# Optimization experiments

Measured on AMD Instinct MI355X. Metric: run time of the kernel, lower is better.

Reference implementation:

```python
import jax, jax.numpy as jnp
import numpy as np

RES = 4096
MAX_VAL = 1.0
COST_SCALE = 0.01
WIDTH = 11
N_ITERS = 20


def setup_inputs() -> dict:
    key = jax.random.key(0)
    k1, k2, k3, k4 = jax.random.split(key, 4)
    x = jax.random.uniform(k1, (RES, RES), jnp.float32)
    bt = jax.random.randint(k2, (RES, RES), 1, 3).astype(jnp.float32)
    sparse = (jax.random.uniform(k4, (RES, RES)) < 0.01).astype(jnp.float32)
    boundary_types = bt * sparse
    boundary_conditions = jax.random.uniform(k3, (RES, RES), jnp.float32) * MAX_VAL
    C = COST_SCALE * jnp.ones((RES, RES), jnp.float32)
    return {"x": x, "boundary_types": boundary_types,
            "boundary_conditions": boundary_conditions, "C": C}


def _neighbor_avg(V):
    # 5-point Jacobi stencil average with edge-replicate boundary handling
    Vp = jnp.pad(V, 1, mode='edge')
    return 0.25 * (Vp[:-2, 1:-1] + Vp[2:, 1:-1] + Vp[1:-1, :-2] + Vp[1:-1, 2:])


def reference(x, boundary_types, boundary_conditions, C):
    obj = boundary_types > 0
    V0 = jnp.where(obj, boundary_conditions, x)
    C_pos = jax.nn.relu(C)

    # dilate object boundary values with a uniform width x width box filter
    objects_bounds = boundary_conditions * (boundary_types == 1) * (boundary_conditions > 0)
    w = jnp.full((1, 1, WIDTH, WIDTH), 1.0 / (WIDTH * WIDTH), jnp.float32)
    extra = jax.lax.conv_general_dilated(
        objects_bounds[None, None], w, window_strides=(1, 1), padding='SAME')[0, 0]
    extra = extra * (boundary_types == 0)
    Cc = C_pos + extra  # effective cost field, shape (RES, RES)

    interior = boundary_types == 0

    def step(V, _):
        Vn = jnp.where(interior, _neighbor_avg(V) + Cc, boundary_conditions)
        return Vn, None

    V, _ = jax.lax.scan(step, V0, None, length=N_ITERS)

    out = jnp.where(V >= MAX_VAL, 0.95 * MAX_VAL, V)
    out = jnp.where(obj, boundary_conditions, out)
    return (out, C_pos)
```

## Files before the change

### kernel.cpp

```cpp
#include <hip/hip_runtime.h>
#include <cstdint>

#define RES 4096
#define N_CELLS (RES*RES)

#define T_STEPS 5
#define OW 64
#define OH 64
#define HALO_V 5
#define HALO_H 8
#define IW (OW + 2*HALO_H)
#define IH (OH + 2*HALO_V)
#define NF4 (IW/4)
#define NSLOT (NF4*IH)
#define NTHR 512
#define LDSW IW
#define BUFSZ (IH*LDSW + 8)
#define K2_LIM (NSLOT - 2*NTHR)

__device__ __forceinline__ void jstep(const float* __restrict__ src,
                                      float* __restrict__ dst,
                                      int lo, int gr, int gc, uint4 pk)
{
    const float4 ctr = *(const float4*)(src + lo);
    const int upo = (gr == 0)     ? lo : lo - LDSW;
    const int dno = (gr == RES-1) ? lo : lo + LDSW;
    const float4 up  = *(const float4*)(src + upo);
    const float4 dn  = *(const float4*)(src + dno);
    const float4 lfq = *(const float4*)(src + (lo - 4));
    const float4 rtq = *(const float4*)(src + (lo + 4));
    const float lf = (gc == 0)         ? ctr.x : lfq.w;
    const float rt = (gc + 3 == RES-1) ? ctr.w : rtq.x;
    float4 nv;
    {   const float m = __uint_as_float(pk.x & 0x7fffffffu);
        const float a = 0.25f*(up.x + dn.x + lf    + ctr.y) + m;
        nv.x = (pk.x >> 31) ? m : a; }
    {   const float m = __uint_as_float(pk.y & 0x7fffffffu);
        const float a = 0.25f*(up.y + dn.y + ctr.x + ctr.z) + m;
        nv.y = (pk.y >> 31) ? m : a; }
    {   const float m = __uint_as_float(pk.z & 0x7fffffffu);
        const float a = 0.25f*(up.z + dn.z + ctr.y + ctr.w) + m;
        nv.z = (pk.z >> 31) ? m : a; }
    {   const float m = __uint_as_float(pk.w & 0x7fffffffu);
        const float a = 0.25f*(up.w + dn.w + ctr.z + rt   ) + m;
        nv.w = (pk.w >> 31) ? m : a; }
    *(float4*)(dst + lo) = nv;
}

__device__ __forceinline__ void stage_slot(const float* __restrict__ Vin,
                                           const uint32_t* __restrict__ packed,
                                           float* __restrict__ bufA,
                                           int idx, int r0, int c0,
                                           int& lo, int& gr, int& gc, uint4& pk)
{
    const int lrow  = idx / NF4;
    const int lcol4 = idx - lrow * NF4;
    gr = r0 - HALO_V + lrow;
    gc = c0 - HALO_H + lcol4 * 4;
    lo = lrow * LDSW + lcol4 * 4;
    float4 vv; uint4 pp;
    const int rr = gr < 0 ? 0 : (gr > RES-1 ? RES-1 : gr);
    if (gc >= 0 && gc + 3 <= RES-1) {
        vv = *(const float4*)(Vin    + (size_t)rr * RES + gc);
        pp = *(const uint4*) (packed + (size_t)rr * RES + gc);
    } else {
#pragma unroll
        for (int e = 0; e < 4; ++e) {
            int cc = gc + e; cc = cc < 0 ? 0 : (cc > RES-1 ? RES-1 : cc);
            ((float*)&vv)[e]    = Vin   [(size_t)rr * RES + cc];
            ((uint32_t*)&pp)[e] = packed[(size_t)rr * RES + cc];
        }
    }
    *(float4*)(bufA + lo) = vv;
    pk = pp;
}

template<int FINAL>
__global__ __launch_bounds__(NTHR, 6) void lap_fused(
    const float* __restrict__ Vin, const uint32_t* __restrict__ packed,
    float* __restrict__ Vout)
{
    __shared__ float lds_raw[2 * BUFSZ];
    float* bufA = lds_raw + 4;
    float* bufB = lds_raw + BUFSZ + 4;
    const int tid = threadIdx.x;
    const int r0 = blockIdx.y * OH;
    const int c0 = blockIdx.x * OW;

    int lo0, gr0, gc0;  uint4 pk0;
    int lo1, gr1, gc1;  uint4 pk1;
    int lo2 = 0, gr2 = 0, gc2 = 0;  uint4 pk2 = {0u,0u,0u,0u};

    stage_slot(Vin, packed, bufA, tid,            r0, c0, lo0, gr0, gc0, pk0);
    stage_slot(Vin, packed, bufA, tid + NTHR,     r0, c0, lo1, gr1, gc1, pk1);
    if (tid < K2_LIM)
        stage_slot(Vin, packed, bufA, tid + 2*NTHR, r0, c0, lo2, gr2, gc2, pk2);
    __syncthreads();

    float* src = bufA;
    float* dst = bufB;
    for (int s = 1; s <= T_STEPS; ++s) {
        const int rlo = (r0 == 0)        ? 0   : (r0 - HALO_V + s);
        const int rhi = (r0 + OH == RES) ? RES : (r0 + OH + HALO_V - s);
        if (gr0 >= rlo && gr0 < rhi) jstep(src, dst, lo0, gr0, gc0, pk0);
        if (gr1 >= rlo && gr1 < rhi) jstep(src, dst, lo1, gr1, gc1, pk1);
        if (tid < K2_LIM && gr2 >= rlo && gr2 < rhi)
                                     jstep(src, dst, lo2, gr2, gc2, pk2);
        __syncthreads();
        float* t = src; src = dst; dst = t;
    }

#define STORE_SLOT(LO, GR, GC, PK, ACT)                                        \
    if ((ACT) && (GR) >= r0 && (GR) < r0 + OH && (GC) >= c0 && (GC) < c0 + OW) {\
        float4 o = *(const float4*)(src + (LO));                               \
        if (FINAL) {                                                           \
            o.x = ((PK).x >> 31) ? o.x : (o.x >= 1.0f ? 0.95f : o.x);          \
            o.y = ((PK).y >> 31) ? o.y : (o.y >= 1.0f ? 0.95f : o.y);          \
            o.z = ((PK).z >> 31) ? o.z : (o.z >= 1.0f ? 0.95f : o.z);          \
            o.w = ((PK).w >> 31) ? o.w : (o.w >= 1.0f ? 0.95f : o.w);          \
        }                                                                      \
        *(float4*)(Vout + (size_t)(GR) * RES + (GC)) = o;                      \
    }
    STORE_SLOT(lo0, gr0, gc0, pk0, true)
    STORE_SLOT(lo1, gr1, gc1, pk1, true)
    STORE_SLOT(lo2, gr2, gc2, pk2, tid < K2_LIM)
#undef STORE_SLOT
}

#define PB_OW 64
#define PB_OH 64
#define PB_HH 8
#define PB_HV 5
#define PB_IW (PB_OW + 2*PB_HH)
#define PB_IH (PB_OH + 2*PB_HV)
#define PB_NF4 (PB_IW/4)
#define PB_NSLOT (PB_NF4*PB_IH)
#define PB_THR 256
#define PB_LDSW 84
#define PB_HLDSW 68

__global__ __launch_bounds__(PB_THR) void lap_precompute(
    const float* __restrict__ x, const float* __restrict__ bt,
    const float* __restrict__ bc, const float* __restrict__ C,
    float* __restrict__ V0, uint32_t* __restrict__ packed)
{
    __shared__ float ob[PB_IH * PB_LDSW];
    __shared__ float hs[PB_IH * PB_HLDSW];
    const int tid = threadIdx.x;
    const int r0 = blockIdx.y * PB_OH, c0 = blockIdx.x * PB_OW;

    for (int idx = tid; idx < PB_NSLOT; idx += PB_THR) {
        const int lrow = idx / PB_NF4;
        const int lcol4 = idx - lrow * PB_NF4;
        const int gr = r0 - PB_HV + lrow;
        const int gc = c0 - PB_HH + lcol4 * 4;
        float4 o = {0.f,0.f,0.f,0.f};
        if (gr >= 0 && gr < RES) {
            if (gc >= 0 && gc + 3 < RES) {
                const float4 b = *(const float4*)(bt + (size_t)gr*RES + gc);
                const float4 w = *(const float4*)(bc + (size_t)gr*RES + gc);
                o.x = (b.x == 1.f && w.x > 0.f) ? w.x : 0.f;
                o.y = (b.y == 1.f && w.y > 0.f) ? w.y : 0.f;
                o.z = (b.z == 1.f && w.z > 0.f) ? w.z : 0.f;
                o.w = (b.w == 1.f && w.w > 0.f) ? w.w : 0.f;
            } else {
#pragma unroll
                for (int e = 0; e < 4; ++e) {
                    const int cc = gc + e;
                    if (cc >= 0 && cc < RES) {
                        const float b = bt[(size_t)gr*RES + cc];
                        const float w = bc[(size_t)gr*RES + cc];
                        ((float*)&o)[e] = (b == 1.f && w > 0.f) ? w : 0.f;
                    }
                }
            }
        }
        *(float4*)(&ob[lrow*PB_LDSW + lcol4*4]) = o;
    }
    __syncthreads();

    for (int idx = tid; idx < PB_IH * 16; idx += PB_THR) {
        const int lrow = idx >> 4;
        const int j4 = (idx & 15) << 2;
        const float* row = &ob[lrow * PB_LDSW];
        const float4 a0 = *(const float4*)(row + j4);
        const float4 a1 = *(const float4*)(row + j4 + 4);
        const float4 a2 = *(const float4*)(row + j4 + 8);
        const float4 a3 = *(const float4*)(row + j4 + 12);
        const float4 a4 = *(const float4*)(row + j4 + 16);
        const float common = a1.z + a1.w + a2.x + a2.y + a2.z + a2.w + a3.x + a3.y;
        float4 s;
        s.x = common + a0.w + a1.x + a1.y;
        s.y = common + a1.x + a1.y + a3.z;
        s.z = common + a1.y + a3.z + a3.w;
        s.w = common + a3.z + a3.w + a4.x;
        *(float4*)(&hs[lrow * PB_HLDSW + j4]) = s;
    }
    __syncthreads();

    for (int idx = tid; idx < PB_OH * 16; idx += PB_THR) {
        const int i = idx >> 4;
        const int j4 = (idx & 15) << 2;
        float sx=0.f, sy=0.f, sz=0.f, sw=0.f;
#pragma unroll
        for (int d = 0; d < 11; ++d) {
            const float4 h = *(const float4*)(&hs[(i + d) * PB_HLDSW + j4]);
            sx += h.x; sy += h.y; sz += h.z; sw += h.w;
        }
        const int gr = r0 + i, gc = c0 + j4;
        const size_t g = (size_t)gr * RES + gc;
        const float4 xx  = *(const float4*)(x  + g);
        const float4 cc  = *(const float4*)(C  + g);
        const float4 btv = *(const float4*)(bt + g);
        const float4 bcv = *(const float4*)(bc + g);
        float4 v0; uint4 pko;
        const float es[4] = {sx, sy, sz, sw};
#pragma unroll
        for (int e = 0; e < 4; ++e) {
            const float cpos = fmaxf(((const float*)&cc)[e], 0.f);
            const bool interior = (((const float*)&btv)[e] == 0.0f);
            const float Cc = cpos + es[e] * (1.0f / 121.0f);
            const float bce = ((const float*)&bcv)[e];
            ((uint32_t*)&pko)[e] = interior ? __float_as_uint(Cc)
                                           : (__float_as_uint(bce) | 0x80000000u);
            ((float*)&v0)[e] = interior ? ((const float*)&xx)[e] : bce;
        }
        *(uint4*)(packed + g) = pko;
        *(float4*)(V0 + g) = v0;
    }
}

__global__ __launch_bounds__(256) void lap_cpos(
    const float* __restrict__ C, float* __restrict__ out2)
{
    const int idx = (blockIdx.x * 256 + threadIdx.x) * 4;
    const float4 c = *(const float4*)(C + idx);
    float4 o;
    o.x = fmaxf(c.x, 0.f); o.y = fmaxf(c.y, 0.f);
    o.z = fmaxf(c.z, 0.f); o.w = fmaxf(c.w, 0.f);
    *(float4*)(out2 + idx) = o;
}

extern "C" void kernel_launch(void* const* d_in, const int* in_sizes, int n_in,
                              void* d_out, int out_size, void* d_ws, size_t ws_size,
                              hipStream_t stream) {
    const float* x  = (const float*)d_in[0];
    const float* bt = (const float*)d_in[1];
    const float* bc = (const float*)d_in[2];
    const float* C  = (const float*)d_in[3];

    float*    out1   = (float*)d_out;
    uint32_t* packed = (uint32_t*)((float*)d_out + N_CELLS);
    float*    vb     = (float*)d_ws;

    dim3 gP(RES / PB_OW, RES / PB_OH);
    lap_precompute<<<gP, PB_THR, 0, stream>>>(x, bt, bc, C, out1, packed);

    dim3 gF(RES / OW, RES / OH);
    lap_fused<0><<<gF, NTHR, 0, stream>>>(out1, packed, vb);
    lap_fused<0><<<gF, NTHR, 0, stream>>>(vb,   packed, out1);
    lap_fused<0><<<gF, NTHR, 0, stream>>>(out1, packed, vb);
    lap_fused<1><<<gF, NTHR, 0, stream>>>(vb,   packed, out1);

    lap_cpos<<<N_CELLS / 1024, 256, 0, stream>>>(C, (float*)d_out + N_CELLS);
}
```

Baseline: 614.6 us.

## Use single in-place LDS buffer for temporal Jacobi steps to raise occupancy

```diff
diff --git a/kernel.cpp b/kernel.cpp
--- a/kernel.cpp
+++ b/kernel.cpp
@@ -18,17 +18,16 @@
 #define BUFSZ (IH*LDSW + 8)
 #define K2_LIM (NSLOT - 2*NTHR)
 
-__device__ __forceinline__ void jstep(const float* __restrict__ src,
-                                      float* __restrict__ dst,
-                                      int lo, int gr, int gc, uint4 pk)
-{
-    const float4 ctr = *(const float4*)(src + lo);
+__device__ __forceinline__ float4 jcalc(const float* buf,
+                                        int lo, int gr, int gc, uint4 pk)
+{
+    const float4 ctr = *(const float4*)(buf + lo);
     const int upo = (gr == 0)     ? lo : lo - LDSW;
     const int dno = (gr == RES-1) ? lo : lo + LDSW;
-    const float4 up  = *(const float4*)(src + upo);
-    const float4 dn  = *(const float4*)(src + dno);
-    const float4 lfq = *(const float4*)(src + (lo - 4));
-    const float4 rtq = *(const float4*)(src + (lo + 4));
+    const float4 up  = *(const float4*)(buf + upo);
+    const float4 dn  = *(const float4*)(buf + dno);
+    const float4 lfq = *(const float4*)(buf + (lo - 4));
+    const float4 rtq = *(const float4*)(buf + (lo + 4));
     const float lf = (gc == 0)         ? ctr.x : lfq.w;
     const float rt = (gc + 3 == RES-1) ? ctr.w : rtq.x;
     float4 nv;
@@ -44,12 +43,12 @@
     {   const float m = __uint_as_float(pk.w & 0x7fffffffu);
         const float a = 0.25f*(up.w + dn.w + ctr.z + rt   ) + m;
         nv.w = (pk.w >> 31) ? m : a; }
-    *(float4*)(dst + lo) = nv;
+    return nv;
 }
 
 __device__ __forceinline__ void stage_slot(const float* __restrict__ Vin,
                                            const uint32_t* __restrict__ packed,
-                                           float* __restrict__ bufA,
+                                           float* buf,
                                            int idx, int r0, int c0,
                                            int& lo, int& gr, int& gc, uint4& pk)
 {
@@ -71,18 +70,17 @@
             ((uint32_t*)&pp)[e] = packed[(size_t)rr * RES + cc];
         }
     }
-    *(float4*)(bufA + lo) = vv;
+    *(float4*)(buf + lo) = vv;
     pk = pp;
 }
 
 template<int FINAL>
-__global__ __launch_bounds__(NTHR, 6) void lap_fused(
+__global__ __launch_bounds__(NTHR, 8) void lap_fused(
     const float* __restrict__ Vin, const uint32_t* __restrict__ packed,
     float* __restrict__ Vout)
 {
-    __shared__ float lds_raw[2 * BUFSZ];
-    float* bufA = lds_raw + 4;
-    float* bufB = lds_raw + BUFSZ + 4;
+    __shared__ float lds_raw[BUFSZ];
+    float* buf = lds_raw + 4;
     const int tid = threadIdx.x;
     const int r0 = blockIdx.y * OH;
     const int c0 = blockIdx.x * OW;
@@ -91,28 +89,32 @@
     int lo1, gr1, gc1;  uint4 pk1;
     int lo2 = 0, gr2 = 0, gc2 = 0;  uint4 pk2 = {0u,0u,0u,0u};
 
-    stage_slot(Vin, packed, bufA, tid,            r0, c0, lo0, gr0, gc0, pk0);
-    stage_slot(Vin, packed, bufA, tid + NTHR,     r0, c0, lo1, gr1, gc1, pk1);
+    stage_slot(Vin, packed, buf, tid,            r0, c0, lo0, gr0, gc0, pk0);
+    stage_slot(Vin, packed, buf, tid + NTHR,     r0, c0, lo1, gr1, gc1, pk1);
     if (tid < K2_LIM)
-        stage_slot(Vin, packed, bufA, tid + 2*NTHR, r0, c0, lo2, gr2, gc2, pk2);
+        stage_slot(Vin, packed, buf, tid + 2*NTHR, r0, c0, lo2, gr2, gc2, pk2);
     __syncthreads();
 
-    float* src = bufA;
-    float* dst = bufB;
-    for (int s = 1; s <= T_STEPS; ++s) {
+    for (int s = 1; s < T_STEPS; ++s) {
         const int rlo = (r0 == 0)        ? 0   : (r0 - HALO_V + s);
         const int rhi = (r0 + OH == RES) ? RES : (r0 + OH + HALO_V - s);
-        if (gr0 >= rlo && gr0 < rhi) jstep(src, dst, lo0, gr0, gc0, pk0);
-        if (gr1 >= rlo && gr1 < rhi) jstep(src, dst, lo1, gr1, gc1, pk1);
-        if (tid < K2_LIM && gr2 >= rlo && gr2 < rhi)
-                                     jstep(src, dst, lo2, gr2, gc2, pk2);
+        const bool a0 = (gr0 >= rlo) && (gr0 < rhi);
+        const bool a1 = (gr1 >= rlo) && (gr1 < rhi);
+        const bool a2 = (tid < K2_LIM) && (gr2 >= rlo) && (gr2 < rhi);
+        float4 nv0, nv1, nv2;
+        if (a0) nv0 = jcalc(buf, lo0, gr0, gc0, pk0);
+        if (a1) nv1 = jcalc(buf, lo1, gr1, gc1, pk1);
+        if (a2) nv2 = jcalc(buf, lo2, gr2, gc2, pk2);
         __syncthreads();
-        float* t = src; src = dst; dst = t;
-    }
-
-#define STORE_SLOT(LO, GR, GC, PK, ACT)                                        \
+        if (a0) *(float4*)(buf + lo0) = nv0;
+        if (a1) *(float4*)(buf + lo1) = nv1;
+        if (a2) *(float4*)(buf + lo2) = nv2;
+        __syncthreads();
+    }
+
+#define FINAL_SLOT(LO, GR, GC, PK, ACT)                                        \
     if ((ACT) && (GR) >= r0 && (GR) < r0 + OH && (GC) >= c0 && (GC) < c0 + OW) {\
-        float4 o = *(const float4*)(src + (LO));                               \
+        float4 o = jcalc(buf, (LO), (GR), (GC), (PK));                         \
         if (FINAL) {                                                           \
             o.x = ((PK).x >> 31) ? o.x : (o.x >= 1.0f ? 0.95f : o.x);          \
             o.y = ((PK).y >> 31) ? o.y : (o.y >= 1.0f ? 0.95f : o.y);          \
@@ -121,10 +123,10 @@
         }                                                                      \
         *(float4*)(Vout + (size_t)(GR) * RES + (GC)) = o;                      \
     }
-    STORE_SLOT(lo0, gr0, gc0, pk0, true)
-    STORE_SLOT(lo1, gr1, gc1, pk1, true)
-    STORE_SLOT(lo2, gr2, gc2, pk2, tid < K2_LIM)
-#undef STORE_SLOT
+    FINAL_SLOT(lo0, gr0, gc0, pk0, true)
+    FINAL_SLOT(lo1, gr1, gc1, pk1, true)
+    FINAL_SLOT(lo2, gr2, gc2, pk2, tid < K2_LIM)
+#undef FINAL_SLOT
 }
 
 #define PB_OW 64
@@ -135,11 +137,11 @@
 #define PB_IH (PB_OH + 2*PB_HV)
 #define PB_NF4 (PB_IW/4)
 #define PB_NSLOT (PB_NF4*PB_IH)
-#define PB_THR 256
+#define PB_THR 512
 #define PB_LDSW 84
 #define PB_HLDSW 68
 
-__global__ __launch_bounds__(PB_THR) void lap_precompute(
+__global__ __launch_bounds__(PB_THR, 6) void lap_precompute(
     const float* __restrict__ x, const float* __restrict__ bt,
     const float* __restrict__ bc, const float* __restrict__ C,
     float* __restrict__ V0, uint32_t* __restrict__ packed)
```

New measurement: 594.9 us. 1.03x faster.
